# Performance work log

Measured on AMD Instinct MI355X. Metric: run time of the kernel, lower is better.

Reference implementation:

```python
import jax, jax.numpy as jnp
import numpy as np


def setup_inputs() -> dict:
    key = jax.random.key(0)
    k1, k2 = jax.random.split(key)
    B, P = 32, 1024
    pred = jax.random.normal(k1, (B, 2 * P), dtype=jnp.float32)
    truth = jax.random.normal(k2, (B, 2 * P), dtype=jnp.float32)
    return {"pred": pred, "truth": truth}


def reference(pred, truth):
    # pred, truth: [B, 2P]; first P cols = X coords, last P = Y coords.
    B = pred.shape[0]
    P = pred.shape[1] // 2
    # diffPred - diffTruth for anchor ix equals d - d[:, ix:ix+1] where d = pred - truth,
    # so the whole loop fuses into one broadcasted pairwise difference.
    d = pred - truth                      # [B, 2P]
    dX, dY = d[:, :P], d[:, P:]

    def per_anchor_dists(v):
        # diff[b, i, j] = v[b, j] - v[b, i]  (i = anchor ix)
        diff = v[:, None, :] - v[:, :, None]          # [B, P, P]
        return jnp.sqrt(jnp.sum(diff * diff, axis=(0, 2)))  # [P] Frobenius dist per ix

    total = jnp.sum(per_anchor_dists(dX)) + jnp.sum(per_anchor_dists(dY))
    return total / (B * 2.0)
```

## Files before the change

### kernel.cpp

```cpp
#include <hip/hip_runtime.h>
#include <math.h>

#define BB 32
#define PP 1024
#define WW 2048
#define MAGIC 0x5CA1AB1Eu

#define WS_S     0
#define WS_SS    64
#define WS_FLAGA 128
#define WS_PART  160
#define WS_FLAGB 192

__device__ __forceinline__ float wave_sum(float v) {
    #pragma unroll
    for (int off = 32; off > 0; off >>= 1)
        v += __shfl_down(v, off, 64);
    return v;
}

__global__ void __launch_bounds__(64)
gcs_one(const float* __restrict__ pred, const float* __restrict__ truth,
        float* __restrict__ out, unsigned* __restrict__ wsu) {
    float* wsf = (float*)wsu;
    const int k    = blockIdx.x;
    const int lane = threadIdx.x;

    #pragma unroll
    for (int h = 0; h < 2; ++h) {
        const float4* p4 = (const float4*)(pred  + k * WW + h * PP);
        const float4* t4 = (const float4*)(truth + k * WW + h * PP);
        float s = 0.f, ss = 0.f;
        #pragma unroll
        for (int j = 0; j < 4; ++j) {
            const float4 a = p4[lane + 64 * j], c = t4[lane + 64 * j];
            const float x0 = a.x - c.x, x1 = a.y - c.y;
            const float x2 = a.z - c.z, x3 = a.w - c.w;
            s  += x0 + x1 + x2 + x3;
            ss += x0 * x0 + x1 * x1 + x2 * x2 + x3 * x3;
        }
        s = wave_sum(s); ss = wave_sum(ss);
        if (lane == 0) {
            __hip_atomic_store(&wsf[WS_S  + h * 32 + k], s,
                               __ATOMIC_RELAXED, __HIP_MEMORY_SCOPE_AGENT);
            __hip_atomic_store(&wsf[WS_SS + h * 32 + k], ss,
                               __ATOMIC_RELAXED, __HIP_MEMORY_SCOPE_AGENT);
        }
    }
    if (lane == 0)
        __hip_atomic_store(&wsu[WS_FLAGA + k], MAGIC,
                           __ATOMIC_RELEASE, __HIP_MEMORY_SCOPE_AGENT);

    const bool need = lane < 32;
    for (;;) {
        const unsigned f = need
            ? __hip_atomic_load(&wsu[WS_FLAGA + lane],
                                __ATOMIC_ACQUIRE, __HIP_MEMORY_SCOPE_AGENT)
            : MAGIC;
        if (__all(f == MAGIC)) break;
    }

    const int a = k * 64 + lane;
    const int h = a >> 10;
    const int i = a & 1023;

    float T = 0.f;
    float Sv[BB];
    #pragma unroll
    for (int b = 0; b < BB; ++b) {
        Sv[b] = __hip_atomic_load(&wsf[WS_S  + h * 32 + b],
                                  __ATOMIC_RELAXED, __HIP_MEMORY_SCOPE_AGENT);
        T    += __hip_atomic_load(&wsf[WS_SS + h * 32 + b],
                                  __ATOMIC_RELAXED, __HIP_MEMORY_SCOPE_AGENT);
    }
    float q = 0.f, r = 0.f;
    #pragma unroll
    for (int b = 0; b < BB; ++b) {
        const int idx = b * WW + h * PP + i;
        const float x = pred[idx] - truth[idx];
        q = fmaf(x, x, q);
        r = fmaf(x, Sv[b], r);
    }
    float si = sqrtf(fmaxf(T + 1024.f * q - 2.f * r, 0.f));
    si = wave_sum(si);
    if (lane == 0) {
        __hip_atomic_store(&wsf[WS_PART + k], si,
                           __ATOMIC_RELAXED, __HIP_MEMORY_SCOPE_AGENT);
        __hip_atomic_store(&wsu[WS_FLAGB + k], MAGIC,
                           __ATOMIC_RELEASE, __HIP_MEMORY_SCOPE_AGENT);
    }

    if (k == 0) {
        for (;;) {
            const unsigned f = need
                ? __hip_atomic_load(&wsu[WS_FLAGB + lane],
                                    __ATOMIC_ACQUIRE, __HIP_MEMORY_SCOPE_AGENT)
                : MAGIC;
            if (__all(f == MAGIC)) break;
        }
        float p = need
            ? __hip_atomic_load(&wsf[WS_PART + lane],
                                __ATOMIC_RELAXED, __HIP_MEMORY_SCOPE_AGENT)
            : 0.f;
        p = wave_sum(p);
        if (lane == 0) out[0] = p * (1.0f / 64.0f);
    }
}

extern "C" void kernel_launch(void* const* d_in, const int* in_sizes, int n_in,
                              void* d_out, int out_size, void* d_ws, size_t ws_size,
                              hipStream_t stream) {
    const float* pred  = (const float*)d_in[0];
    const float* truth = (const float*)d_in[1];
    gcs_one<<<32, 64, 0, stream>>>(pred, truth, (float*)d_out, (unsigned*)d_ws);
}
```

Before: 59.80 us.

## Recompute per-row sums per block to drop the first grid-wide barrier

Each block now computes the per-row sum and sum-of-squares for its whole half in shared memory, instead of publishing them through workspace flags and spinning on a grid-wide barrier. Blocks grow from 64 to 256 threads: four waves split the batch rows and their partial q/r values are combined through shared memory. This removes one cross-block spin-wait and its atomic traffic. The cost is redundant reads of the half's data in every block, served mostly from L2, plus two block-level syncs.

```diff
diff --git a/kernel.cpp b/kernel.cpp
--- a/kernel.cpp
+++ b/kernel.cpp
@@ -6,11 +6,8 @@
 #define WW 2048
 #define MAGIC 0x5CA1AB1Eu
 
-#define WS_S     0
-#define WS_SS    64
-#define WS_FLAGA 128
-#define WS_PART  160
-#define WS_FLAGB 192
+#define WS_PART 0
+#define WS_FLAG 32
 
 __device__ __forceinline__ float wave_sum(float v) {
     #pragma unroll
@@ -19,91 +16,84 @@
     return v;
 }
 
-__global__ void __launch_bounds__(64)
+__global__ void __launch_bounds__(256)
 gcs_one(const float* __restrict__ pred, const float* __restrict__ truth,
         float* __restrict__ out, unsigned* __restrict__ wsu) {
     float* wsf = (float*)wsu;
     const int k    = blockIdx.x;
-    const int lane = threadIdx.x;
+    const int h    = k >> 4;
+    const int t    = threadIdx.x;
+    const int wave = t >> 6;
+    const int lane = t & 63;
+
+    __shared__ float S[BB], SQ[BB];
+    __shared__ float qbuf[4][64], rbuf[4][64];
 
     #pragma unroll
-    for (int h = 0; h < 2; ++h) {
-        const float4* p4 = (const float4*)(pred  + k * WW + h * PP);
-        const float4* t4 = (const float4*)(truth + k * WW + h * PP);
+    for (int j = 0; j < 8; ++j) {
+        const int b = 4 * j + wave;
+        const float4* p4 = (const float4*)(pred  + b * WW + h * PP);
+        const float4* t4 = (const float4*)(truth + b * WW + h * PP);
         float s = 0.f, ss = 0.f;
         #pragma unroll
-        for (int j = 0; j < 4; ++j) {
-            const float4 a = p4[lane + 64 * j], c = t4[lane + 64 * j];
+        for (int m = 0; m < 4; ++m) {
+            const float4 a = p4[lane + 64 * m], c = t4[lane + 64 * m];
             const float x0 = a.x - c.x, x1 = a.y - c.y;
             const float x2 = a.z - c.z, x3 = a.w - c.w;
-            s  += x0 + x1 + x2 + x3;
+            s  += (x0 + x1) + (x2 + x3);
             ss += x0 * x0 + x1 * x1 + x2 * x2 + x3 * x3;
         }
         s = wave_sum(s); ss = wave_sum(ss);
-        if (lane == 0) {
-            __hip_atomic_store(&wsf[WS_S  + h * 32 + k], s,
-                               __ATOMIC_RELAXED, __HIP_MEMORY_SCOPE_AGENT);
-            __hip_atomic_store(&wsf[WS_SS + h * 32 + k], ss,
-                               __ATOMIC_RELAXED, __HIP_MEMORY_SCOPE_AGENT);
-        }
+        if (lane == 0) { S[b] = s; SQ[b] = ss; }
     }
-    if (lane == 0)
-        __hip_atomic_store(&wsu[WS_FLAGA + k], MAGIC,
-                           __ATOMIC_RELEASE, __HIP_MEMORY_SCOPE_AGENT);
-
-    const bool need = lane < 32;
-    for (;;) {
-        const unsigned f = need
-            ? __hip_atomic_load(&wsu[WS_FLAGA + lane],
-                                __ATOMIC_ACQUIRE, __HIP_MEMORY_SCOPE_AGENT)
-            : MAGIC;
-        if (__all(f == MAGIC)) break;
-    }
-
-    const int a = k * 64 + lane;
-    const int h = a >> 10;
-    const int i = a & 1023;
+    __syncthreads();
 
     float T = 0.f;
-    float Sv[BB];
     #pragma unroll
-    for (int b = 0; b < BB; ++b) {
-        Sv[b] = __hip_atomic_load(&wsf[WS_S  + h * 32 + b],
-                                  __ATOMIC_RELAXED, __HIP_MEMORY_SCOPE_AGENT);
-        T    += __hip_atomic_load(&wsf[WS_SS + h * 32 + b],
-                                  __ATOMIC_RELAXED, __HIP_MEMORY_SCOPE_AGENT);
-    }
+    for (int b = 0; b < BB; ++b) T += SQ[b];
+
+    const int i = (k & 15) * 64 + lane;
     float q = 0.f, r = 0.f;
     #pragma unroll
-    for (int b = 0; b < BB; ++b) {
+    for (int jj = 0; jj < 8; ++jj) {
+        const int b = wave * 8 + jj;
         const int idx = b * WW + h * PP + i;
         const float x = pred[idx] - truth[idx];
         q = fmaf(x, x, q);
-        r = fmaf(x, Sv[b], r);
+        r = fmaf(x, S[b], r);
     }
-    float si = sqrtf(fmaxf(T + 1024.f * q - 2.f * r, 0.f));
-    si = wave_sum(si);
-    if (lane == 0) {
-        __hip_atomic_store(&wsf[WS_PART + k], si,
-                           __ATOMIC_RELAXED, __HIP_MEMORY_SCOPE_AGENT);
-        __hip_atomic_store(&wsu[WS_FLAGB + k], MAGIC,
-                           __ATOMIC_RELEASE, __HIP_MEMORY_SCOPE_AGENT);
-    }
+    qbuf[wave][lane] = q; rbuf[wave][lane] = r;
+    __syncthreads();
 
-    if (k == 0) {
-        for (;;) {
-            const unsigned f = need
-                ? __hip_atomic_load(&wsu[WS_FLAGB + lane],
-                                    __ATOMIC_ACQUIRE, __HIP_MEMORY_SCOPE_AGENT)
-                : MAGIC;
-            if (__all(f == MAGIC)) break;
+    if (wave == 0) {
+        q = (qbuf[0][lane] + qbuf[1][lane]) + (qbuf[2][lane] + qbuf[3][lane]);
+        r = (rbuf[0][lane] + rbuf[1][lane]) + (rbuf[2][lane] + rbuf[3][lane]);
+        float si = sqrtf(fmaxf(T + 1024.f * q - 2.f * r, 0.f));
+        si = wave_sum(si);
+        if (lane == 0) {
+            __hip_atomic_store(&wsf[WS_PART + k], si,
+                               __ATOMIC_RELAXED, __HIP_MEMORY_SCOPE_AGENT);
+            __hip_atomic_store(&wsu[WS_FLAG + k], MAGIC,
+                               __ATOMIC_RELEASE, __HIP_MEMORY_SCOPE_AGENT);
         }
-        float p = need
-            ? __hip_atomic_load(&wsf[WS_PART + lane],
-                                __ATOMIC_RELAXED, __HIP_MEMORY_SCOPE_AGENT)
-            : 0.f;
-        p = wave_sum(p);
-        if (lane == 0) out[0] = p * (1.0f / 64.0f);
+
+        if (k == 0) {
+            const bool need = lane < 32;
+            for (;;) {
+                const unsigned f = need
+                    ? __hip_atomic_load(&wsu[WS_FLAG + lane],
+                                        __ATOMIC_ACQUIRE,
+                                        __HIP_MEMORY_SCOPE_AGENT)
+                    : MAGIC;
+                if (__all(f == MAGIC)) break;
+            }
+            float p = need
+                ? __hip_atomic_load(&wsf[WS_PART + lane],
+                                    __ATOMIC_RELAXED, __HIP_MEMORY_SCOPE_AGENT)
+                : 0.f;
+            p = wave_sum(p);
+            if (lane == 0) out[0] = p * (1.0f / 64.0f);
+        }
     }
 }
 
@@ -112,5 +102,5 @@
                               hipStream_t stream) {
     const float* pred  = (const float*)d_in[0];
     const float* truth = (const float*)d_in[1];
-    gcs_one<<<32, 64, 0, stream>>>(pred, truth, (float*)d_out, (unsigned*)d_ws);
+    gcs_one<<<32, 256, 0, stream>>>(pred, truth, (float*)d_out, (unsigned*)d_ws);
 }
```

Result: slower. 62.23 us (+4.0%).
